# Optimization experiments

Hardware: AMD Instinct MI355X
Metric: run time of the kernel (lower is better)

The kernel has to match this reference:

```python
import jax, jax.numpy as jnp
import numpy as np

# Model dims (eval mode: dropout off, no gate noise, no KV cache, start_pos=0)
B, T, C = 2, 2048, 1024
H, KV = 16, 4
HD = C // H            # 64
E, K = 8, 2            # n_experts, active_experts
FE, FS = 1024, 2048    # expert_inter_dim, shared inter_dim
EPS = 1e-6
BASE = 10000.0


def setup_inputs() -> dict:
    key = jax.random.key(0)
    ks = jax.random.split(key, 15)
    s = 0.02
    f32 = jnp.float32
    return {
        'x': jax.random.normal(ks[0], (B, T, C), f32),
        'norm1_w': jnp.ones((C,), f32),
        'norm2_w': jnp.ones((C,), f32),
        'wq': jax.random.normal(ks[1], (C, H * HD), f32) * s,
        'wk': jax.random.normal(ks[2], (C, KV * HD), f32) * s,
        'wv': jax.random.normal(ks[3], (C, KV * HD), f32) * s,
        'wo': jax.random.normal(ks[4], (H * HD, C), f32) * s,
        'gate_w': jax.random.normal(ks[5], (C, E), f32) * s,
        'exp_w1': jax.random.normal(ks[6], (E, C, FE), f32) * s,
        'exp_w2': jax.random.normal(ks[7], (E, C, FE), f32) * s,
        'exp_wp': jax.random.normal(ks[8], (E, FE, C), f32) * s,
        'sh_w1': jax.random.normal(ks[9], (C, FS), f32) * s,
        'sh_w2': jax.random.normal(ks[10], (C, FS), f32) * s,
        'sh_wp': jax.random.normal(ks[11], (FS, C), f32) * s,
    }


def _rms(x, w):
    return x * jax.lax.rsqrt(jnp.mean(x * x, -1, keepdims=True) + EPS) * w


def _rope_table(t, hd):
    freqs = 1.0 / (BASE ** (jnp.arange(0, hd, 2, dtype=jnp.float32) / hd))
    ang = jnp.outer(jnp.arange(t, dtype=jnp.float32), freqs)  # (T, hd/2)
    return jnp.stack([jnp.cos(ang), jnp.sin(ang)], -1)        # (T, hd/2, 2)


def _apply_rope(x, fc):
    # x: (B, T, nH, hd); fc: (T, hd/2, 2)
    xr = x.reshape(*x.shape[:-1], -1, 2)
    cos = fc[None, :, None, :, 0]
    sin = fc[None, :, None, :, 1]
    out = jnp.stack([xr[..., 0] * cos - xr[..., 1] * sin,
                     xr[..., 1] * cos + xr[..., 0] * sin], -1)
    return out.reshape(x.shape).astype(x.dtype)


def reference(x, norm1_w, norm2_w, wq, wk, wv, wo, gate_w,
              exp_w1, exp_w2, exp_wp, sh_w1, sh_w2, sh_wp):
    fc = _rope_table(T, HD)
    # --- GQA attention with RoPE ---
    h1 = _rms(x, norm1_w)
    q = (h1 @ wq).reshape(B, T, H, HD)
    k = (h1 @ wk).reshape(B, T, KV, HD)
    v = (h1 @ wv).reshape(B, T, KV, HD)
    q = _apply_rope(q, fc)
    k = _apply_rope(k, fc)
    rep = H // KV
    k = jnp.repeat(k, rep, axis=2)  # (B,T,H,HD)
    v = jnp.repeat(v, rep, axis=2)
    scores = jnp.einsum('bqhd,bkhd->bhqk', q, k) / jnp.sqrt(jnp.float32(HD))
    mask = jnp.where(jnp.tril(jnp.ones((T, T), bool)), 0.0, -1e9).astype(scores.dtype)
    att = jax.nn.softmax(scores + mask, axis=-1)
    o = jnp.einsum('bhqk,bkhd->bqhd', att, v).reshape(B, T, C) @ wo
    x1 = x + o
    # --- MoE block (top-k gate, dense masked combine == gather/scatter math) ---
    h2 = _rms(x1, norm2_w).reshape(-1, C)  # (N, C), N = B*T
    gate_logits = h2 @ gate_w              # (N, E)
    p = jax.nn.softmax(gate_logits, axis=-1)
    topw, topi = jax.lax.top_k(p, K)       # values == gather(p, indices)
    comb = jnp.sum(jax.nn.one_hot(topi, E, dtype=p.dtype) * topw[..., None], axis=1)  # (N, E)
    he = jax.nn.silu(jnp.einsum('nc,ecf->enf', h2, exp_w1)) * jnp.einsum('nc,ecf->enf', h2, exp_w2)
    ye = jnp.einsum('enf,efc->enc', he, exp_wp)
    y = jnp.einsum('enc,ne->nc', ye, comb)
    z = (jax.nn.silu(h2 @ sh_w1) * (h2 @ sh_w2)) @ sh_wp
    out = x1 + (y + z).reshape(B, T, C)
    return out, gate_logits
```

## Files before the change

kernel.cpp:

```cpp
#include <hip/hip_runtime.h>
#include <hip/hip_bf16.h>

#define TB 2
#define TT 2048
#define TC 1024
#define TH 16
#define TKV 4
#define THD 64
#define TE 8
#define TFE 1024
#define TFS 2048
#define NTOK 4096
#define NSLOT 8192

typedef __attribute__((ext_vector_type(4))) float f32x4;
typedef __attribute__((ext_vector_type(8))) short s16x8;

__device__ __forceinline__ float bf2f(short s) {
    unsigned int u = ((unsigned int)(unsigned short)s) << 16;
    return __builtin_bit_cast(float, u);
}
__device__ __forceinline__ short f2bf(float f) {
    unsigned int u = __builtin_bit_cast(unsigned int, f);
    u = u + 0x7fffu + ((u >> 16) & 1u);
    return (short)(u >> 16);
}

__device__ __forceinline__ void gl_lds16(const void* g, void* l) {
    __builtin_amdgcn_global_load_lds((const __attribute__((address_space(1))) void*)g,
                                     (__attribute__((address_space(3))) void*)l,
                                     16, 0, 0);
}

__global__ __launch_bounds__(256) void k_transp(const float* __restrict__ in,
                                                short* __restrict__ out,
                                                int R, int Cd,
                                                size_t bs_in, size_t bs_out) {
    __shared__ float tile[32][33];
    const float* ip = in + bs_in * blockIdx.z;
    short* op = out + bs_out * blockIdx.z;
    int tx = threadIdx.x & 31, ty = threadIdx.x >> 5;
    int r0 = blockIdx.y * 32, c0 = blockIdx.x * 32;
    #pragma unroll
    for (int r = ty; r < 32; r += 8)
        tile[r][tx] = ip[(size_t)(r0 + r) * Cd + c0 + tx];
    __syncthreads();
    #pragma unroll
    for (int r = ty; r < 32; r += 8)
        op[(size_t)(c0 + r) * R + r0 + tx] = f2bf(tile[tx][r]);
}

__global__ __launch_bounds__(256) void k_transp_v(const short* __restrict__ qkv,
                                                  short* __restrict__ v_t) {
    __shared__ short tile[32][33];
    int z = blockIdx.z;
    int b = z >> 2, kvh = z & 3;
    const short* ip = qkv + (size_t)b * TT * 1536 + 1280 + kvh * 64;
    short* op = v_t + (size_t)z * THD * TT;
    int tx = threadIdx.x & 31, ty = threadIdx.x >> 5;
    int t0 = blockIdx.y * 32, d0 = blockIdx.x * 32;
    #pragma unroll
    for (int r = ty; r < 32; r += 8)
        tile[r][tx] = ip[(size_t)(t0 + r) * 1536 + d0 + tx];
    __syncthreads();
    #pragma unroll
    for (int r = ty; r < 32; r += 8)
        op[(size_t)(d0 + r) * TT + t0 + tx] = tile[tx][r];
}

__global__ void k_rope_table(float* __restrict__ rope) {
    int idx = blockIdx.x * 256 + threadIdx.x;
    if (idx >= TT * 32) return;
    int t = idx >> 5, i = idx & 31;
    float freq = expf(-(float)i * (1.0f / 32.0f) * 9.210340371976184f);
    float ang = (float)t * freq;
    rope[idx * 2 + 0] = cosf(ang);
    rope[idx * 2 + 1] = sinf(ang);
}

__global__ __launch_bounds__(256) void k_rmsnorm(const float* __restrict__ x,
                                                 const float* __restrict__ w,
                                                 short* __restrict__ out) {
    int row = blockIdx.x, t = threadIdx.x;
    float4 v = ((const float4*)(x + (size_t)row * TC))[t];
    float ss = v.x * v.x + v.y * v.y + v.z * v.z + v.w * v.w;
    #pragma unroll
    for (int off = 32; off; off >>= 1) ss += __shfl_xor(ss, off);
    __shared__ float red[4];
    if ((t & 63) == 0) red[t >> 6] = ss;
    __syncthreads();
    float rs = rsqrtf((red[0] + red[1] + red[2] + red[3]) * (1.0f / 1024.0f) + 1e-6f);
    float4 wv = ((const float4*)w)[t];
    short4 o;
    o.x = f2bf(v.x * rs * wv.x);
    o.y = f2bf(v.y * rs * wv.y);
    o.z = f2bf(v.z * rs * wv.z);
    o.w = f2bf(v.w * rs * wv.w);
    ((short4*)(out + (size_t)row * TC))[t] = o;
}

template <int EPI>
__global__ __launch_bounds__(256) void k_gemm128(const short* __restrict__ A,
                                                 const short* __restrict__ Bt,
                                                 void* __restrict__ outp,
                                                 const float* __restrict__ resid,
                                                 int M, int N, int K) {
    __shared__ short As[128 * 32];
    __shared__ short Bs[128 * 32];
    int tid = threadIdx.x;
    int brow = blockIdx.y * 128, bcol = blockIdx.x * 128;
    int wid = tid >> 6, lane = tid & 63;
    int wr = wid >> 1, wc = wid & 1, g = lane >> 4, c = lane & 15;
    int srow = wid * 32 + (lane >> 2);
    int scol = (lane & 3) * 8;
    const short* Ag0 = A + (size_t)(brow + srow) * K + scol;
    const short* Ag1 = A + (size_t)(brow + srow + 16) * K + scol;
    const short* Bg0 = Bt + (size_t)(bcol + srow) * K + scol;
    const short* Bg1 = Bt + (size_t)(bcol + srow + 16) * K + scol;
    int loff = __builtin_amdgcn_readfirstlane(wid * 2048);
    char* Al0 = (char*)As + loff;
    char* Bl0 = (char*)Bs + loff;
    f32x4 acc[4][4] = {};
    for (int kk = 0; kk < K; kk += 32) {
        __syncthreads();
        gl_lds16(Ag0 + kk, Al0);
        gl_lds16(Ag1 + kk, Al0 + 1024);
        gl_lds16(Bg0 + kk, Bl0);
        gl_lds16(Bg1 + kk, Bl0 + 1024);
        __syncthreads();
        s16x8 af[4], bf[4];
        #pragma unroll
        for (int m = 0; m < 4; m++) af[m] = *(const s16x8*)(As + (wr * 64 + m * 16 + c) * 32 + g * 8);
        #pragma unroll
        for (int n = 0; n < 4; n++) bf[n] = *(const s16x8*)(Bs + (wc * 64 + n * 16 + c) * 32 + g * 8);
        #pragma unroll
        for (int m = 0; m < 4; m++)
            #pragma unroll
            for (int n = 0; n < 4; n++)
                acc[m][n] = __builtin_amdgcn_mfma_f32_16x16x32_bf16(af[m], bf[n], acc[m][n], 0, 0, 0);
    }
    #pragma unroll
    for (int m = 0; m < 4; m++)
        #pragma unroll
        for (int n = 0; n < 4; n++)
            #pragma unroll
            for (int j = 0; j < 4; j++) {
                int row = brow + wr * 64 + m * 16 + g * 4 + j;
                int col = bcol + wc * 64 + n * 16 + c;
                float v = acc[m][n][j];
                if (EPI == 0)
                    ((short*)outp)[(size_t)row * N + col] = f2bf(v);
                else
                    ((float*)outp)[(size_t)row * N + col] = v + resid[(size_t)row * N + col];
            }
}

__global__ void k_rope_apply(const short* __restrict__ qkv,
                             const float* __restrict__ rope,
                             short* __restrict__ q_r,
                             short* __restrict__ k_r) {
    int idx = blockIdx.x * 256 + threadIdx.x;
    if (idx >= NTOK * 640) return;
    int row = idx / 640;
    int p = idx - row * 640;
    int b = row >> 11, t = row & 2047;
    const short* src = qkv + (size_t)row * 1536;
    if (p < 512) {
        int h = p >> 5, i = p & 31;
        float x0 = bf2f(src[h * 64 + 2 * i]);
        float x1 = bf2f(src[h * 64 + 2 * i + 1]);
        float cs = rope[(t * 32 + i) * 2], sn = rope[(t * 32 + i) * 2 + 1];
        size_t o = ((size_t)(b * TH + h) * TT + t) * THD + 2 * i;
        q_r[o]     = f2bf(x0 * cs - x1 * sn);
        q_r[o + 1] = f2bf(x1 * cs + x0 * sn);
    } else {
        int pk = p - 512;
        int kv = pk >> 5, i = pk & 31;
        float x0 = bf2f(src[1024 + kv * 64 + 2 * i]);
        float x1 = bf2f(src[1024 + kv * 64 + 2 * i + 1]);
        float cs = rope[(t * 32 + i) * 2], sn = rope[(t * 32 + i) * 2 + 1];
        size_t o = ((size_t)(b * TKV + kv) * TT + t) * THD + 2 * i;
        k_r[o]     = f2bf(x0 * cs - x1 * sn);
        k_r[o + 1] = f2bf(x1 * cs + x0 * sn);
    }
}

__global__ __launch_bounds__(256) void k_attn(const short* __restrict__ q_r,
                                              const short* __restrict__ k_r,
                                              const short* __restrict__ v_t,
                                              short* __restrict__ attn_o) {
    int qb = (TT / 64 - 1) - blockIdx.x;
    int bh = blockIdx.y;
    int b = bh >> 4, h = bh & 15, kv = h >> 2;
    int tid = threadIdx.x;
    int w = tid >> 6, lane = tid & 63, g = lane >> 4, c = lane & 15;
    int qrow = qb * 64 + w * 16;

    const short* qp = q_r + ((size_t)(b * TH + h) * TT + qrow) * THD;
    const short* kp = k_r + ((size_t)(b * TKV + kv) * TT) * THD;
    const short* vp = v_t + ((size_t)(b * TKV + kv) * THD) * TT;

    s16x8 aq[2];
    aq[0] = *(const s16x8*)(qp + c * THD + g * 8);
    aq[1] = *(const s16x8*)(qp + c * THD + 32 + g * 8);

    f32x4 o[4] = {};
    float m[4]  = {-1e30f, -1e30f, -1e30f, -1e30f};
    float lsum[4] = {0.f, 0.f, 0.f, 0.f};

    __shared__ short pbuf[4][16 * 64];
    short* pb = &pbuf[w][0];

    s16x8 kcur[8], knext[8], vf[8];
    #pragma unroll
    for (int nt = 0; nt < 4; nt++) {
        kcur[nt * 2]     = *(const s16x8*)(kp + (nt * 16 + c) * THD + g * 8);
        kcur[nt * 2 + 1] = *(const s16x8*)(kp + (nt * 16 + c) * THD + 32 + g * 8);
    }

    for (int kt = 0; kt <= qb; ++kt) {
        #pragma unroll
        for (int nt = 0; nt < 4; nt++) {
            vf[nt * 2]     = *(const s16x8*)(vp + (size_t)(nt * 16 + c) * TT + kt * 64 + g * 8);
            vf[nt * 2 + 1] = *(const s16x8*)(vp + (size_t)(nt * 16 + c) * TT + kt * 64 + 32 + g * 8);
        }
        {
            int ktn = kt < qb ? kt + 1 : kt;
            const short* kpn = kp + (size_t)ktn * 64 * THD;
            #pragma unroll
            for (int nt = 0; nt < 4; nt++) {
                knext[nt * 2]     = *(const s16x8*)(kpn + (nt * 16 + c) * THD + g * 8);
                knext[nt * 2 + 1] = *(const s16x8*)(kpn + (nt * 16 + c) * THD + 32 + g * 8);
            }
        }
        f32x4 S[4] = {};
        #pragma unroll
        for (int nt = 0; nt < 4; nt++) {
            S[nt] = __builtin_amdgcn_mfma_f32_16x16x32_bf16(aq[0], kcur[nt * 2], S[nt], 0, 0, 0);
            S[nt] = __builtin_amdgcn_mfma_f32_16x16x32_bf16(aq[1], kcur[nt * 2 + 1], S[nt], 0, 0, 0);
        }
        #pragma unroll
        for (int nt = 0; nt < 4; nt++)
            #pragma unroll
            for (int j = 0; j < 4; j++) {
                float s = S[nt][j] * 0.125f;
                if (kt == qb) {
                    int kpos = nt * 16 + c;
                    int qpos = w * 16 + g * 4 + j;
                    if (kpos > qpos) s = -1e30f;
                }
                S[nt][j] = s;
            }
        float mn[4];
        #pragma unroll
        for (int j = 0; j < 4; j++) {
            mn[j] = fmaxf(fmaxf(S[0][j], S[1][j]), fmaxf(S[2][j], S[3][j]));
            mn[j] = fmaxf(mn[j], __shfl_xor(mn[j], 1));
            mn[j] = fmaxf(mn[j], __shfl_xor(mn[j], 2));
            mn[j] = fmaxf(mn[j], __shfl_xor(mn[j], 4));
            mn[j] = fmaxf(mn[j], __shfl_xor(mn[j], 8));
        }
        #pragma unroll
        for (int j = 0; j < 4; j++) {
            float mnew = fmaxf(m[j], mn[j]);
            float al = __expf(m[j] - mnew);
            m[j] = mnew;
            lsum[j] *= al;
            #pragma unroll
            for (int nt = 0; nt < 4; nt++) o[nt][j] *= al;
        }
        float rsum[4] = {0.f, 0.f, 0.f, 0.f};
        #pragma unroll
        for (int nt = 0; nt < 4; nt++)
            #pragma unroll
            for (int j = 0; j < 4; j++) {
                float pv = __expf(S[nt][j] - m[j]);
                S[nt][j] = pv;
                rsum[j] += pv;
            }
        #pragma unroll
        for (int j = 0; j < 4; j++) {
            rsum[j] += __shfl_xor(rsum[j], 1);
            rsum[j] += __shfl_xor(rsum[j], 2);
            rsum[j] += __shfl_xor(rsum[j], 4);
            rsum[j] += __shfl_xor(rsum[j], 8);
            lsum[j] += rsum[j];
        }
        #pragma unroll
        for (int nt = 0; nt < 4; nt++)
            #pragma unroll
            for (int j = 0; j < 4; j++) {
                int row = g * 4 + j;
                pb[(row * 64 + nt * 16 + c) ^ ((row & 7) << 3)] = f2bf(S[nt][j]);
            }
        s16x8 pa0 = *(const s16x8*)(pb + ((c * 64 + g * 8) ^ ((c & 7) << 3)));
        s16x8 pa1 = *(const s16x8*)(pb + ((c * 64 + 32 + g * 8) ^ ((c & 7) << 3)));
        #pragma unroll
        for (int nt = 0; nt < 4; nt++) {
            o[nt] = __builtin_amdgcn_mfma_f32_16x16x32_bf16(pa0, vf[nt * 2], o[nt], 0, 0, 0);
            o[nt] = __builtin_amdgcn_mfma_f32_16x16x32_bf16(pa1, vf[nt * 2 + 1], o[nt], 0, 0, 0);
        }
        #pragma unroll
        for (int i = 0; i < 8; i++) kcur[i] = knext[i];
    }
    float inv[4];
    #pragma unroll
    for (int j = 0; j < 4; j++) inv[j] = 1.0f / lsum[j];
    #pragma unroll
    for (int nt = 0; nt < 4; nt++)
        #pragma unroll
        for (int j = 0; j < 4; j++) {
            float v = o[nt][j] * inv[j];
            attn_o[(size_t)(b * TT + qb * 64 + w * 16 + g * 4 + j) * TC + h * THD + nt * 16 + c] = f2bf(v);
        }
    (void)qrow;
}

__global__ __launch_bounds__(256) void k_gate(const float* __restrict__ x1,
                                              const float* __restrict__ n2w,
                                              const float* __restrict__ gate_w,
                                              float* __restrict__ gl,
                                              int* __restrict__ cnt,
                                              int* __restrict__ te,
                                              int* __restrict__ tls,
                                              float* __restrict__ tw) {
    int w = threadIdx.x >> 6, lane = threadIdx.x & 63;
    int n = blockIdx.x * 4 + w;
    const float* xp = x1 + (size_t)n * TC;
    float ss = 0.f;
    for (int i = lane; i < TC; i += 64) { float v = xp[i]; ss += v * v; }
    #pragma unroll
    for (int off = 32; off; off >>= 1) ss += __shfl_xor(ss, off);
    float rs = rsqrtf(ss * (1.0f / 1024.0f) + 1e-6f);
    int e = lane & 7, ch = lane >> 3;
    float acc = 0.f;
    for (int i = 0; i < 128; i++) {
        int cc = ch * 128 + i;
        acc += xp[cc] * rs * n2w[cc] * gate_w[(size_t)cc * TE + e];
    }
    acc += __shfl_xor(acc, 8);
    acc += __shfl_xor(acc, 16);
    acc += __shfl_xor(acc, 32);
    float logit = acc;
    if (lane < 8) gl[(size_t)n * TE + lane] = logit;
    float mx = logit;
    mx = fmaxf(mx, __shfl_xor(mx, 1)); mx = fmaxf(mx, __shfl_xor(mx, 2)); mx = fmaxf(mx, __shfl_xor(mx, 4));
    float ex = __expf(logit - mx);
    float sm = ex;
    sm += __shfl_xor(sm, 1); sm += __shfl_xor(sm, 2); sm += __shfl_xor(sm, 4);
    float pp = ex / sm;
    float m1 = pp;
    m1 = fmaxf(m1, __shfl_xor(m1, 1)); m1 = fmaxf(m1, __shfl_xor(m1, 2)); m1 = fmaxf(m1, __shfl_xor(m1, 4));
    int cand = (pp == m1) ? e : 8;
    int e0 = cand;
    e0 = min(e0, __shfl_xor(e0, 1)); e0 = min(e0, __shfl_xor(e0, 2)); e0 = min(e0, __shfl_xor(e0, 4));
    float p2 = (e == e0) ? -1.0f : pp;
    float m2 = p2;
    m2 = fmaxf(m2, __shfl_xor(m2, 1)); m2 = fmaxf(m2, __shfl_xor(m2, 2)); m2 = fmaxf(m2, __shfl_xor(m2, 4));
    int cand2 = (p2 == m2) ? e : 8;
    int e1 = cand2;
    e1 = min(e1, __shfl_xor(e1, 1)); e1 = min(e1, __shfl_xor(e1, 2)); e1 = min(e1, __shfl_xor(e1, 4));
    if (lane == 0) {
        int ls0 = atomicAdd(&cnt[e0], 1);
        int ls1 = atomicAdd(&cnt[e1], 1);
        te[n * 2] = e0; te[n * 2 + 1] = e1;
        tls[n * 2] = ls0; tls[n * 2 + 1] = ls1;
        tw[n * 2] = m1; tw[n * 2 + 1] = m2;
    }
}

__global__ void k_prefix(const int* __restrict__ cnt, int* __restrict__ basep) {
    if (threadIdx.x == 0) {
        int s = 0;
        for (int e = 0; e < TE; e++) { basep[e] = s; s += cnt[e]; }
    }
}

__global__ void k_scatter(const int* __restrict__ te, const int* __restrict__ tls,
                          const float* __restrict__ tw, const int* __restrict__ basep,
                          int* __restrict__ tlist, float* __restrict__ slotw,
                          int* __restrict__ sot) {
    int n = blockIdx.x * 256 + threadIdx.x;
    if (n >= NTOK) return;
    int s0 = basep[te[n * 2]] + tls[n * 2];
    int s1 = basep[te[n * 2 + 1]] + tls[n * 2 + 1];
    tlist[s0] = n; tlist[s1] = n;
    slotw[s0] = tw[n * 2]; slotw[s1] = tw[n * 2 + 1];
    sot[n * 2] = s0; sot[n * 2 + 1] = s1;
}

template <int GATHER>
__global__ __launch_bounds__(256) void k_dual(const short* __restrict__ A,
                                              const short* __restrict__ B1t,
                                              const short* __restrict__ B2t,
                                              short* __restrict__ Out,
                                              const int* __restrict__ cnt,
                                              const int* __restrict__ basep,
                                              const int* __restrict__ tlist,
                                              const float* __restrict__ slotw,
                                              size_t wrows, int ldout, int K) {
    int e = blockIdx.z;
    int mt = blockIdx.y, nt = blockIdx.x;
    int ce = 0, base = 0;
    if (GATHER) {
        ce = cnt[e];
        if (mt * 128 >= ce) return;
        base = basep[e];
    }
    __shared__ short As[128 * 32];
    __shared__ short B1s[64 * 32];
    __shared__ short B2s[64 * 32];
    int tid = threadIdx.x, wid = tid >> 6, lane = tid & 63;
    int wr = wid >> 1, wc = wid & 1, g = lane >> 4, c = lane & 15;
    int srow = wid * 32 + (lane >> 2);
    int scol = (lane & 3) * 8;
    size_t arow0, arow1;
    if (GATHER) {
        int l0 = mt * 128 + srow;      if (l0 >= ce) l0 = ce - 1;
        int l1 = mt * 128 + srow + 16; if (l1 >= ce) l1 = ce - 1;
        arow0 = (size_t)tlist[base + l0];
        arow1 = (size_t)tlist[base + l1];
    } else {
        arow0 = (size_t)(mt * 128 + srow);
        arow1 = arow0 + 16;
    }
    const short* Ag0 = A + arow0 * (size_t)K + scol;
    const short* Ag1 = A + arow1 * (size_t)K + scol;
    int brow_s = wid * 16 + (lane >> 2);
    const short* B1g = B1t + ((size_t)e * wrows + (size_t)(nt * 64 + brow_s)) * K + scol;
    const short* B2g = B2t + ((size_t)e * wrows + (size_t)(nt * 64 + brow_s)) * K + scol;
    int loffA = __builtin_amdgcn_readfirstlane(wid * 2048);
    int loffB = __builtin_amdgcn_readfirstlane(wid * 1024);
    char* Al = (char*)As + loffA;
    char* B1l = (char*)B1s + loffB;
    char* B2l = (char*)B2s + loffB;
    f32x4 a1[4][2] = {}, a2[4][2] = {};
    for (int kk = 0; kk < K; kk += 32) {
        __syncthreads();
        gl_lds16(Ag0 + kk, Al);
        gl_lds16(Ag1 + kk, Al + 1024);
        gl_lds16(B1g + kk, B1l);
        gl_lds16(B2g + kk, B2l);
        __syncthreads();
        s16x8 af[4], b1[2], b2[2];
        #pragma unroll
        for (int m_ = 0; m_ < 4; m_++) af[m_] = *(const s16x8*)(As + (wr * 64 + m_ * 16 + c) * 32 + g * 8);
        #pragma unroll
        for (int n = 0; n < 2; n++) {
            b1[n] = *(const s16x8*)(B1s + (wc * 32 + n * 16 + c) * 32 + g * 8);
            b2[n] = *(const s16x8*)(B2s + (wc * 32 + n * 16 + c) * 32 + g * 8);
        }
        #pragma unroll
        for (int m_ = 0; m_ < 4; m_++)
            #pragma unroll
            for (int n = 0; n < 2; n++) {
                a1[m_][n] = __builtin_amdgcn_mfma_f32_16x16x32_bf16(af[m_], b1[n], a1[m_][n], 0, 0, 0);
                a2[m_][n] = __builtin_amdgcn_mfma_f32_16x16x32_bf16(af[m_], b2[n], a2[m_][n], 0, 0, 0);
            }
    }
    #pragma unroll
    for (int m_ = 0; m_ < 4; m_++)
        #pragma unroll
        for (int n = 0; n < 2; n++)
            #pragma unroll
            for (int j = 0; j < 4; j++) {
                int lrow = mt * 128 + wr * 64 + m_ * 16 + g * 4 + j;
                if (GATHER && lrow >= ce) continue;
                int col = nt * 64 + wc * 32 + n * 16 + c;
                float g1 = a1[m_][n][j], g2 = a2[m_][n][j];
                float v = g1 / (1.0f + __expf(-g1)) * g2;
                size_t orow = GATHER ? (size_t)(base + lrow) : (size_t)lrow;
                if (GATHER) v *= slotw[base + lrow];
                Out[orow * (size_t)ldout + col] = f2bf(v);
            }
}

__global__ __launch_bounds__(256) void k_moe2(const short* __restrict__ he,
                                              const short* __restrict__ Wpt,
                                              short* __restrict__ ye,
                                              const int* __restrict__ cnt,
                                              const int* __restrict__ basep) {
    int e = blockIdx.z;
    int ce = cnt[e];
    int mt = blockIdx.y;
    if (mt * 128 >= ce) return;
    int base = basep[e];
    int nt = blockIdx.x;
    __shared__ short As[128 * 32];
    __shared__ short Bs[128 * 32];
    int tid = threadIdx.x, wid = tid >> 6, lane = tid & 63;
    int wr = wid >> 1, wc = wid & 1, g = lane >> 4, c = lane & 15;
    int srow = wid * 32 + (lane >> 2);
    int scol = (lane & 3) * 8;
    const short* Ag0 = he + (size_t)(base + mt * 128 + srow) * TFE + scol;
    const short* Ag1 = Ag0 + (size_t)16 * TFE;
    const short* Bg0 = Wpt + ((size_t)e * 1024 + nt * 128 + srow) * TFE + scol;
    const short* Bg1 = Bg0 + (size_t)16 * TFE;
    int loff = __builtin_amdgcn_readfirstlane(wid * 2048);
    char* Al = (char*)As + loff;
    char* Bl = (char*)Bs + loff;
    f32x4 acc[4][4] = {};
    for (int kk = 0; kk < TFE; kk += 32) {
        __syncthreads();
        gl_lds16(Ag0 + kk, Al);
        gl_lds16(Ag1 + kk, Al + 1024);
        gl_lds16(Bg0 + kk, Bl);
        gl_lds16(Bg1 + kk, Bl + 1024);
        __syncthreads();
        s16x8 af[4], bf[4];
        #pragma unroll
        for (int m = 0; m < 4; m++) af[m] = *(const s16x8*)(As + (wr * 64 + m * 16 + c) * 32 + g * 8);
        #pragma unroll
        for (int n = 0; n < 4; n++) bf[n] = *(const s16x8*)(Bs + (wc * 64 + n * 16 + c) * 32 + g * 8);
        #pragma unroll
        for (int m = 0; m < 4; m++)
            #pragma unroll
            for (int n = 0; n < 4; n++)
                acc[m][n] = __builtin_amdgcn_mfma_f32_16x16x32_bf16(af[m], bf[n], acc[m][n], 0, 0, 0);
    }
    #pragma unroll
    for (int m = 0; m < 4; m++)
        #pragma unroll
        for (int n = 0; n < 4; n++)
            #pragma unroll
            for (int j = 0; j < 4; j++) {
                int lrow = mt * 128 + wr * 64 + m * 16 + g * 4 + j;
                if (lrow >= ce) continue;
                int col = nt * 128 + wc * 64 + n * 16 + c;
                ye[(size_t)(base + lrow) * TC + col] = f2bf(acc[m][n][j]);
            }
}

__global__ __launch_bounds__(256) void k_final(const short* __restrict__ A,
                                               const short* __restrict__ Bt,
                                               const float* __restrict__ x1,
                                               const short* __restrict__ ye,
                                               const int* __restrict__ sot,
                                               float* __restrict__ outp) {
    __shared__ short As[128 * 32];
    __shared__ short Bs[128 * 32];
    const int K = TFS;
    int tid = threadIdx.x;
    int brow = blockIdx.y * 128, bcol = blockIdx.x * 128;
    int wid = tid >> 6, lane = tid & 63;
    int wr = wid >> 1, wc = wid & 1, g = lane >> 4, c = lane & 15;
    int srow = wid * 32 + (lane >> 2);
    int scol = (lane & 3) * 8;
    const short* Ag0 = A + (size_t)(brow + srow) * K + scol;
    const short* Ag1 = A + (size_t)(brow + srow + 16) * K + scol;
    const short* Bg0 = Bt + (size_t)(bcol + srow) * K + scol;
    const short* Bg1 = Bt + (size_t)(bcol + srow + 16) * K + scol;
    int loff = __builtin_amdgcn_readfirstlane(wid * 2048);
    char* Al = (char*)As + loff;
    char* Bl = (char*)Bs + loff;
    f32x4 acc[4][4] = {};
    for (int kk = 0; kk < K; kk += 32) {
        __syncthreads();
        gl_lds16(Ag0 + kk, Al);
        gl_lds16(Ag1 + kk, Al + 1024);
        gl_lds16(Bg0 + kk, Bl);
        gl_lds16(Bg1 + kk, Bl + 1024);
        __syncthreads();
        s16x8 af[4], bf[4];
        #pragma unroll
        for (int m = 0; m < 4; m++) af[m] = *(const s16x8*)(As + (wr * 64 + m * 16 + c) * 32 + g * 8);
        #pragma unroll
        for (int n = 0; n < 4; n++) bf[n] = *(const s16x8*)(Bs + (wc * 64 + n * 16 + c) * 32 + g * 8);
        #pragma unroll
        for (int m = 0; m < 4; m++)
            #pragma unroll
            for (int n = 0; n < 4; n++)
                acc[m][n] = __builtin_amdgcn_mfma_f32_16x16x32_bf16(af[m], bf[n], acc[m][n], 0, 0, 0);
    }
    #pragma unroll
    for (int m = 0; m < 4; m++)
        #pragma unroll
        for (int n = 0; n < 4; n++)
            #pragma unroll
            for (int j = 0; j < 4; j++) {
                int row = brow + wr * 64 + m * 16 + g * 4 + j;
                int col = bcol + wc * 64 + n * 16 + c;
                int s0 = sot[row * 2], s1 = sot[row * 2 + 1];
                float v = acc[m][n][j] + x1[(size_t)row * TC + col]
                        + bf2f(ye[(size_t)s0 * TC + col]) + bf2f(ye[(size_t)s1 * TC + col]);
                outp[(size_t)row * TC + col] = v;
            }
}

extern "C" void kernel_launch(void* const* d_in, const int* in_sizes, int n_in,
                              void* d_out, int out_size, void* d_ws, size_t ws_size,
                              hipStream_t stream) {
    const float* x     = (const float*)d_in[0];
    const float* n1w   = (const float*)d_in[1];
    const float* n2w   = (const float*)d_in[2];
    const float* wq    = (const float*)d_in[3];
    const float* wk    = (const float*)d_in[4];
    const float* wv    = (const float*)d_in[5];
    const float* wo    = (const float*)d_in[6];
    const float* gatew = (const float*)d_in[7];
    const float* ew1   = (const float*)d_in[8];
    const float* ew2   = (const float*)d_in[9];
    const float* ewp   = (const float*)d_in[10];
    const float* sw1   = (const float*)d_in[11];
    const float* sw2   = (const float*)d_in[12];
    const float* swp   = (const float*)d_in[13];
    float* outp = (float*)d_out;

    char* p = (char*)d_ws;
    auto alloc = [&](size_t bytes) -> char* {
        char* r = p;
        p += (bytes + 255) & ~(size_t)255;
        return r;
    };
    short* wqkv_t = (short*)alloc(1536 * 1024 * 2);
    short* wo_t   = (short*)alloc(1024 * 1024 * 2);
    short* ew1_t  = (short*)alloc((size_t)8 * 1024 * 1024 * 2);
    short* ew2_t  = (short*)alloc((size_t)8 * 1024 * 1024 * 2);
    short* ewp_t  = (short*)alloc((size_t)8 * 1024 * 1024 * 2);
    short* sw1_t  = (short*)alloc((size_t)2048 * 1024 * 2);
    short* sw2_t  = (short*)alloc((size_t)2048 * 1024 * 2);
    short* swp_t  = (short*)alloc((size_t)1024 * 2048 * 2);
    short* h1     = (short*)alloc((size_t)NTOK * 1024 * 2);
    short* qkv    = (short*)alloc((size_t)NTOK * 1536 * 2);
    short* q_r    = (short*)alloc((size_t)TB * TH * TT * THD * 2);
    short* k_r    = (short*)alloc((size_t)TB * TKV * TT * THD * 2);
    short* v_t    = (short*)alloc((size_t)TB * TKV * THD * TT * 2);
    short* attn_o = (short*)alloc((size_t)NTOK * 1024 * 2);
    float* x1     = (float*)alloc((size_t)NTOK * 1024 * 4);
    short* h2     = (short*)alloc((size_t)NTOK * 1024 * 2);
    float* rope   = (float*)alloc((size_t)TT * 32 * 2 * 4);
    int*   cnt    = (int*)alloc(256);
    int*   basep  = (int*)alloc(256);
    int*   te     = (int*)alloc((size_t)NTOK * 2 * 4);
    int*   tls    = (int*)alloc((size_t)NTOK * 2 * 4);
    float* tw     = (float*)alloc((size_t)NTOK * 2 * 4);
    int*   tlist  = (int*)alloc((size_t)NSLOT * 4);
    float* slotw  = (float*)alloc((size_t)NSLOT * 4);
    int*   sot    = (int*)alloc((size_t)NTOK * 2 * 4);
    short* he     = (short*)alloc((size_t)NSLOT * TFE * 2);
    short* ye     = (short*)alloc((size_t)NSLOT * TC * 2);
    short* shm    = (short*)alloc((size_t)NTOK * TFS * 2);

    dim3 blk(256);

    k_transp<<<dim3(32, 32, 1), blk, 0, stream>>>(wq, wqkv_t, 1024, 1024, 0, 0);
    k_transp<<<dim3(8, 32, 1), blk, 0, stream>>>(wk, wqkv_t + 1024 * 1024, 1024, 256, 0, 0);
    k_transp<<<dim3(8, 32, 1), blk, 0, stream>>>(wv, wqkv_t + 1280 * 1024, 1024, 256, 0, 0);
    k_transp<<<dim3(32, 32, 1), blk, 0, stream>>>(wo, wo_t, 1024, 1024, 0, 0);
    k_transp<<<dim3(32, 32, 8), blk, 0, stream>>>(ew1, ew1_t, 1024, 1024, 1048576, 1048576);
    k_transp<<<dim3(32, 32, 8), blk, 0, stream>>>(ew2, ew2_t, 1024, 1024, 1048576, 1048576);
    k_transp<<<dim3(32, 32, 8), blk, 0, stream>>>(ewp, ewp_t, 1024, 1024, 1048576, 1048576);
    k_transp<<<dim3(64, 32, 1), blk, 0, stream>>>(sw1, sw1_t, 1024, 2048, 0, 0);
    k_transp<<<dim3(64, 32, 1), blk, 0, stream>>>(sw2, sw2_t, 1024, 2048, 0, 0);
    k_transp<<<dim3(32, 64, 1), blk, 0, stream>>>(swp, swp_t, 2048, 1024, 0, 0);

    k_rope_table<<<(TT * 32 + 255) / 256, blk, 0, stream>>>(rope);

    k_rmsnorm<<<NTOK, blk, 0, stream>>>(x, n1w, h1);
    k_gemm128<0><<<dim3(12, 32), blk, 0, stream>>>(h1, wqkv_t, qkv, nullptr, NTOK, 1536, 1024);
    k_rope_apply<<<(NTOK * 640 + 255) / 256, blk, 0, stream>>>(qkv, rope, q_r, k_r);
    k_transp_v<<<dim3(2, 64, 8), blk, 0, stream>>>(qkv, v_t);

    k_attn<<<dim3(TT / 64, TB * TH), blk, 0, stream>>>(q_r, k_r, v_t, attn_o);

    k_gemm128<1><<<dim3(8, 32), blk, 0, stream>>>(attn_o, wo_t, x1, x, NTOK, 1024, 1024);

    k_rmsnorm<<<NTOK, blk, 0, stream>>>(x1, n2w, h2);

    hipMemsetAsync(cnt, 0, 64, stream);
    k_gate<<<NTOK / 4, blk, 0, stream>>>(x1, n2w, gatew, outp + (size_t)NTOK * TC, cnt, te, tls, tw);
    k_prefix<<<1, 64, 0, stream>>>(cnt, basep);
    k_scatter<<<NTOK / 256, blk, 0, stream>>>(te, tls, tw, basep, tlist, slotw, sot);

    k_dual<1><<<dim3(16, 32, 8), blk, 0, stream>>>(h2, ew1_t, ew2_t, he, cnt, basep, tlist, slotw,
                                                   1024, TFE, 1024);
    k_moe2<<<dim3(8, 32, 8), blk, 0, stream>>>(he, ewp_t, ye, cnt, basep);

    k_dual<0><<<dim3(32, 32, 1), blk, 0, stream>>>(h2, sw1_t, sw2_t, shm, nullptr, nullptr, nullptr,
                                                   nullptr, 0, TFS, 1024);

    k_final<<<dim3(8, 32), blk, 0, stream>>>(shm, swp_t, x1, ye, sot, outp);

    (void)in_sizes; (void)n_in; (void)out_size; (void)ws_size;
}
```

Before: 846.9 us.

## Rewrite attention with 32x32 MFMA, shrink GEMM N-tiles, merge FFN launches

Attention now gives each wave its own 32-query tile. It uses 32x32x16 bf16 MFMAs, keeps probabilities in registers through cvt_pk_bf16 and permlane32_swap instead of an LDS round trip, and raises MFMA issue priority. The dense GEMMs (QKV, Wo, MoE down projection, final) move from 128x128 to 128x64 tiles, doubling the block count to fill more CUs. The MoE up-projection and the shared-expert up-projection are merged into one launch so they overlap. This trades per-block data reuse and makes more early-exiting blocks in the merged grid in exchange for higher occupancy and no LDS traffic in attention.

```diff
diff --git a/kernel.cpp b/kernel.cpp
--- a/kernel.cpp
+++ b/kernel.cpp
@@ -14,6 +14,7 @@
 #define NSLOT 8192
 
 typedef __attribute__((ext_vector_type(4))) float f32x4;
+typedef __attribute__((ext_vector_type(16))) float f32x16;
 typedef __attribute__((ext_vector_type(8))) short s16x8;
 
 __device__ __forceinline__ float bf2f(short s) {
@@ -24,6 +25,11 @@
     unsigned int u = __builtin_bit_cast(unsigned int, f);
     u = u + 0x7fffu + ((u >> 16) & 1u);
     return (short)(u >> 16);
+}
+__device__ __forceinline__ unsigned int cvtpk_bf16(float lo, float hi) {
+    unsigned int r;
+    asm volatile("v_cvt_pk_bf16_f32 %0, %1, %2" : "=v"(r) : "v"(lo), "v"(hi));
+    return r;
 }
 
 __device__ __forceinline__ void gl_lds16(const void* g, void* l) {
@@ -100,53 +106,53 @@
 }
 
 template <int EPI>
-__global__ __launch_bounds__(256) void k_gemm128(const short* __restrict__ A,
-                                                 const short* __restrict__ Bt,
-                                                 void* __restrict__ outp,
-                                                 const float* __restrict__ resid,
-                                                 int M, int N, int K) {
+__global__ __launch_bounds__(256) void k_gemm64(const short* __restrict__ A,
+                                                const short* __restrict__ Bt,
+                                                void* __restrict__ outp,
+                                                const float* __restrict__ resid,
+                                                int M, int N, int K) {
     __shared__ short As[128 * 32];
-    __shared__ short Bs[128 * 32];
+    __shared__ short Bs[64 * 32];
     int tid = threadIdx.x;
-    int brow = blockIdx.y * 128, bcol = blockIdx.x * 128;
+    int brow = blockIdx.y * 128, bcol = blockIdx.x * 64;
     int wid = tid >> 6, lane = tid & 63;
     int wr = wid >> 1, wc = wid & 1, g = lane >> 4, c = lane & 15;
     int srow = wid * 32 + (lane >> 2);
     int scol = (lane & 3) * 8;
     const short* Ag0 = A + (size_t)(brow + srow) * K + scol;
     const short* Ag1 = A + (size_t)(brow + srow + 16) * K + scol;
-    const short* Bg0 = Bt + (size_t)(bcol + srow) * K + scol;
-    const short* Bg1 = Bt + (size_t)(bcol + srow + 16) * K + scol;
-    int loff = __builtin_amdgcn_readfirstlane(wid * 2048);
-    char* Al0 = (char*)As + loff;
-    char* Bl0 = (char*)Bs + loff;
-    f32x4 acc[4][4] = {};
+    int sbrow = wid * 16 + (lane >> 2);
+    const short* Bg = Bt + (size_t)(bcol + sbrow) * K + scol;
+    int loffA = __builtin_amdgcn_readfirstlane(wid * 2048);
+    int loffB = __builtin_amdgcn_readfirstlane(wid * 1024);
+    char* Al = (char*)As + loffA;
+    char* Bl = (char*)Bs + loffB;
+    f32x4 acc[4][2] = {};
     for (int kk = 0; kk < K; kk += 32) {
         __syncthreads();
-        gl_lds16(Ag0 + kk, Al0);
-        gl_lds16(Ag1 + kk, Al0 + 1024);
-        gl_lds16(Bg0 + kk, Bl0);
-        gl_lds16(Bg1 + kk, Bl0 + 1024);
-        __syncthreads();
-        s16x8 af[4], bf[4];
+        gl_lds16(Ag0 + kk, Al);
+        gl_lds16(Ag1 + kk, Al + 1024);
+        gl_lds16(Bg + kk, Bl);
+        __syncthreads();
+        s16x8 af[4], bf[2];
         #pragma unroll
         for (int m = 0; m < 4; m++) af[m] = *(const s16x8*)(As + (wr * 64 + m * 16 + c) * 32 + g * 8);
         #pragma unroll
-        for (int n = 0; n < 4; n++) bf[n] = *(const s16x8*)(Bs + (wc * 64 + n * 16 + c) * 32 + g * 8);
+        for (int n = 0; n < 2; n++) bf[n] = *(const s16x8*)(Bs + (wc * 32 + n * 16 + c) * 32 + g * 8);
         #pragma unroll
         for (int m = 0; m < 4; m++)
             #pragma unroll
-            for (int n = 0; n < 4; n++)
+            for (int n = 0; n < 2; n++)
                 acc[m][n] = __builtin_amdgcn_mfma_f32_16x16x32_bf16(af[m], bf[n], acc[m][n], 0, 0, 0);
     }
     #pragma unroll
     for (int m = 0; m < 4; m++)
         #pragma unroll
-        for (int n = 0; n < 4; n++)
+        for (int n = 0; n < 2; n++)
             #pragma unroll
             for (int j = 0; j < 4; j++) {
                 int row = brow + wr * 64 + m * 16 + g * 4 + j;
-                int col = bcol + wc * 64 + n * 16 + c;
+                int col = bcol + wc * 32 + n * 16 + c;
                 float v = acc[m][n][j];
                 if (EPI == 0)
                     ((short*)outp)[(size_t)row * N + col] = f2bf(v);
@@ -189,131 +195,121 @@
                                               const short* __restrict__ k_r,
                                               const short* __restrict__ v_t,
                                               short* __restrict__ attn_o) {
-    int qb = (TT / 64 - 1) - blockIdx.x;
+    int w = threadIdx.x >> 6, lane = threadIdx.x & 63;
+    int qt = 63 - (blockIdx.x * 4 + w);
+    int qbase = qt * 32;
     int bh = blockIdx.y;
     int b = bh >> 4, h = bh & 15, kv = h >> 2;
-    int tid = threadIdx.x;
-    int w = tid >> 6, lane = tid & 63, g = lane >> 4, c = lane & 15;
-    int qrow = qb * 64 + w * 16;
-
-    const short* qp = q_r + ((size_t)(b * TH + h) * TT + qrow) * THD;
+    int q32 = lane & 31, hi = lane >> 5;
+
+    const short* qp = q_r + ((size_t)(b * TH + h) * TT + qbase) * THD;
     const short* kp = k_r + ((size_t)(b * TKV + kv) * TT) * THD;
     const short* vp = v_t + ((size_t)(b * TKV + kv) * THD) * TT;
 
-    s16x8 aq[2];
-    aq[0] = *(const s16x8*)(qp + c * THD + g * 8);
-    aq[1] = *(const s16x8*)(qp + c * THD + 32 + g * 8);
-
-    f32x4 o[4] = {};
-    float m[4]  = {-1e30f, -1e30f, -1e30f, -1e30f};
-    float lsum[4] = {0.f, 0.f, 0.f, 0.f};
-
-    __shared__ short pbuf[4][16 * 64];
-    short* pb = &pbuf[w][0];
-
-    s16x8 kcur[8], knext[8], vf[8];
-    #pragma unroll
-    for (int nt = 0; nt < 4; nt++) {
-        kcur[nt * 2]     = *(const s16x8*)(kp + (nt * 16 + c) * THD + g * 8);
-        kcur[nt * 2 + 1] = *(const s16x8*)(kp + (nt * 16 + c) * THD + 32 + g * 8);
-    }
-
-    for (int kt = 0; kt <= qb; ++kt) {
-        #pragma unroll
-        for (int nt = 0; nt < 4; nt++) {
-            vf[nt * 2]     = *(const s16x8*)(vp + (size_t)(nt * 16 + c) * TT + kt * 64 + g * 8);
-            vf[nt * 2 + 1] = *(const s16x8*)(vp + (size_t)(nt * 16 + c) * TT + kt * 64 + 32 + g * 8);
-        }
-        {
-            int ktn = kt < qb ? kt + 1 : kt;
-            const short* kpn = kp + (size_t)ktn * 64 * THD;
-            #pragma unroll
-            for (int nt = 0; nt < 4; nt++) {
-                knext[nt * 2]     = *(const s16x8*)(kpn + (nt * 16 + c) * THD + g * 8);
-                knext[nt * 2 + 1] = *(const s16x8*)(kpn + (nt * 16 + c) * THD + 32 + g * 8);
+    s16x8 qf[4];
+    #pragma unroll
+    for (int dc = 0; dc < 4; dc++)
+        qf[dc] = *(const s16x8*)(qp + q32 * THD + dc * 16 + hi * 8);
+
+    f32x16 ot0 = {}, ot1 = {};
+    float mrun = -1e30f, lrun = 0.f;
+    int nkt = (qbase + 95) >> 6;
+
+    for (int kt = 0; kt < nkt; kt++) {
+        int ktb = kt * 64;
+        f32x16 st0 = {}, st1 = {};
+        s16x8 kf0[4], kf1[4];
+        #pragma unroll
+        for (int dc = 0; dc < 4; dc++) {
+            kf0[dc] = *(const s16x8*)(kp + (size_t)(ktb + q32) * THD + dc * 16 + hi * 8);
+            kf1[dc] = *(const s16x8*)(kp + (size_t)(ktb + 32 + q32) * THD + dc * 16 + hi * 8);
+        }
+        s16x8 vf[8];
+        #pragma unroll
+        for (int dt = 0; dt < 2; dt++)
+            #pragma unroll
+            for (int kc = 0; kc < 4; kc++)
+                vf[dt * 4 + kc] = *(const s16x8*)(vp + (size_t)(dt * 32 + q32) * TT + ktb + kc * 16 + hi * 8);
+
+        __builtin_amdgcn_s_setprio(1);
+        #pragma unroll
+        for (int dc = 0; dc < 4; dc++) {
+            st0 = __builtin_amdgcn_mfma_f32_32x32x16_bf16(kf0[dc], qf[dc], st0, 0, 0, 0);
+            st1 = __builtin_amdgcn_mfma_f32_32x32x16_bf16(kf1[dc], qf[dc], st1, 0, 0, 0);
+        }
+        __builtin_amdgcn_s_setprio(0);
+
+        bool domask = (kt == nkt - 1);
+        int qabs = qbase + q32;
+        #pragma unroll
+        for (int r = 0; r < 16; r++) {
+            int kploc = (r & 3) + 8 * (r >> 2) + 4 * hi;
+            float s0 = st0[r] * 0.125f;
+            float s1 = st1[r] * 0.125f;
+            if (domask) {
+                if (ktb + kploc > qabs) s0 = -1e30f;
+                if (ktb + 32 + kploc > qabs) s1 = -1e30f;
             }
-        }
-        f32x4 S[4] = {};
-        #pragma unroll
-        for (int nt = 0; nt < 4; nt++) {
-            S[nt] = __builtin_amdgcn_mfma_f32_16x16x32_bf16(aq[0], kcur[nt * 2], S[nt], 0, 0, 0);
-            S[nt] = __builtin_amdgcn_mfma_f32_16x16x32_bf16(aq[1], kcur[nt * 2 + 1], S[nt], 0, 0, 0);
-        }
-        #pragma unroll
-        for (int nt = 0; nt < 4; nt++)
-            #pragma unroll
-            for (int j = 0; j < 4; j++) {
-                float s = S[nt][j] * 0.125f;
-                if (kt == qb) {
-                    int kpos = nt * 16 + c;
-                    int qpos = w * 16 + g * 4 + j;
-                    if (kpos > qpos) s = -1e30f;
-                }
-                S[nt][j] = s;
-            }
-        float mn[4];
-        #pragma unroll
-        for (int j = 0; j < 4; j++) {
-            mn[j] = fmaxf(fmaxf(S[0][j], S[1][j]), fmaxf(S[2][j], S[3][j]));
-            mn[j] = fmaxf(mn[j], __shfl_xor(mn[j], 1));
-            mn[j] = fmaxf(mn[j], __shfl_xor(mn[j], 2));
-            mn[j] = fmaxf(mn[j], __shfl_xor(mn[j], 4));
-            mn[j] = fmaxf(mn[j], __shfl_xor(mn[j], 8));
-        }
-        #pragma unroll
-        for (int j = 0; j < 4; j++) {
-            float mnew = fmaxf(m[j], mn[j]);
-            float al = __expf(m[j] - mnew);
-            m[j] = mnew;
-            lsum[j] *= al;
-            #pragma unroll
-            for (int nt = 0; nt < 4; nt++) o[nt][j] *= al;
-        }
-        float rsum[4] = {0.f, 0.f, 0.f, 0.f};
-        #pragma unroll
-        for (int nt = 0; nt < 4; nt++)
-            #pragma unroll
-            for (int j = 0; j < 4; j++) {
-                float pv = __expf(S[nt][j] - m[j]);
-                S[nt][j] = pv;
-                rsum[j] += pv;
-            }
-        #pragma unroll
-        for (int j = 0; j < 4; j++) {
-            rsum[j] += __shfl_xor(rsum[j], 1);
-            rsum[j] += __shfl_xor(rsum[j], 2);
-            rsum[j] += __shfl_xor(rsum[j], 4);
-            rsum[j] += __shfl_xor(rsum[j], 8);
-            lsum[j] += rsum[j];
-        }
-        #pragma unroll
-        for (int nt = 0; nt < 4; nt++)
-            #pragma unroll
-            for (int j = 0; j < 4; j++) {
-                int row = g * 4 + j;
-                pb[(row * 64 + nt * 16 + c) ^ ((row & 7) << 3)] = f2bf(S[nt][j]);
-            }
-        s16x8 pa0 = *(const s16x8*)(pb + ((c * 64 + g * 8) ^ ((c & 7) << 3)));
-        s16x8 pa1 = *(const s16x8*)(pb + ((c * 64 + 32 + g * 8) ^ ((c & 7) << 3)));
-        #pragma unroll
-        for (int nt = 0; nt < 4; nt++) {
-            o[nt] = __builtin_amdgcn_mfma_f32_16x16x32_bf16(pa0, vf[nt * 2], o[nt], 0, 0, 0);
-            o[nt] = __builtin_amdgcn_mfma_f32_16x16x32_bf16(pa1, vf[nt * 2 + 1], o[nt], 0, 0, 0);
-        }
-        #pragma unroll
-        for (int i = 0; i < 8; i++) kcur[i] = knext[i];
-    }
-    float inv[4];
-    #pragma unroll
-    for (int j = 0; j < 4; j++) inv[j] = 1.0f / lsum[j];
-    #pragma unroll
-    for (int nt = 0; nt < 4; nt++)
-        #pragma unroll
-        for (int j = 0; j < 4; j++) {
-            float v = o[nt][j] * inv[j];
-            attn_o[(size_t)(b * TT + qb * 64 + w * 16 + g * 4 + j) * TC + h * THD + nt * 16 + c] = f2bf(v);
-        }
-    (void)qrow;
+            st0[r] = s0; st1[r] = s1;
+        }
+        float pm = st0[0];
+        #pragma unroll
+        for (int r = 1; r < 16; r++) pm = fmaxf(pm, st0[r]);
+        #pragma unroll
+        for (int r = 0; r < 16; r++) pm = fmaxf(pm, st1[r]);
+        pm = fmaxf(pm, __shfl_xor(pm, 32));
+        float mnew = fmaxf(mrun, pm);
+        float al = __expf(mrun - mnew);
+        mrun = mnew;
+        float rs = 0.f;
+        #pragma unroll
+        for (int r = 0; r < 16; r++) {
+            float e0 = __expf(st0[r] - mnew); st0[r] = e0; rs += e0;
+            float e1 = __expf(st1[r] - mnew); st1[r] = e1; rs += e1;
+        }
+        rs += __shfl_xor(rs, 32);
+        lrun = lrun * al + rs;
+        #pragma unroll
+        for (int r = 0; r < 16; r++) { ot0[r] *= al; ot1[r] *= al; }
+
+        unsigned int w0[8], w1[8];
+        #pragma unroll
+        for (int j = 0; j < 8; j++) {
+            w0[j] = cvtpk_bf16(st0[2 * j], st0[2 * j + 1]);
+            w1[j] = cvtpk_bf16(st1[2 * j], st1[2 * j + 1]);
+        }
+        s16x8 pf[4];
+        #pragma unroll
+        for (int kc = 0; kc < 4; kc++) {
+            unsigned int* ww = (kc < 2) ? w0 : w1;
+            int kcl = kc & 1;
+            unsigned int x0 = ww[4 * kcl + 0], y0 = ww[4 * kcl + 2];
+            unsigned int x1 = ww[4 * kcl + 1], y1 = ww[4 * kcl + 3];
+            asm volatile("v_permlane32_swap_b32 %0, %1" : "+v"(x0), "+v"(y0));
+            asm volatile("v_permlane32_swap_b32 %0, %1" : "+v"(x1), "+v"(y1));
+            unsigned int fr[4] = {x0, x1, y0, y1};
+            pf[kc] = __builtin_bit_cast(s16x8, *(ulong2*)fr);
+        }
+        __builtin_amdgcn_s_setprio(1);
+        #pragma unroll
+        for (int kc = 0; kc < 4; kc++) {
+            ot0 = __builtin_amdgcn_mfma_f32_32x32x16_bf16(vf[kc], pf[kc], ot0, 0, 0, 0);
+            ot1 = __builtin_amdgcn_mfma_f32_32x32x16_bf16(vf[4 + kc], pf[kc], ot1, 0, 0, 0);
+        }
+        __builtin_amdgcn_s_setprio(0);
+    }
+    float inv = 1.0f / lrun;
+    short* orow = attn_o + (size_t)(b * TT + qbase + q32) * TC + h * THD;
+    #pragma unroll
+    for (int s = 0; s < 4; s++) {
+        short4 v0, v1;
+        v0.x = f2bf(ot0[4 * s + 0] * inv); v0.y = f2bf(ot0[4 * s + 1] * inv);
+        v0.z = f2bf(ot0[4 * s + 2] * inv); v0.w = f2bf(ot0[4 * s + 3] * inv);
+        v1.x = f2bf(ot1[4 * s + 0] * inv); v1.y = f2bf(ot1[4 * s + 1] * inv);
+        v1.z = f2bf(ot1[4 * s + 2] * inv); v1.w = f2bf(ot1[4 * s + 3] * inv);
+        *(short4*)(orow + 8 * s + 4 * hi) = v0;
+        *(short4*)(orow + 32 + 8 * s + 4 * hi) = v1;
+    }
 }
 
 __global__ __launch_bounds__(256) void k_gate(const float* __restrict__ x1,
@@ -389,33 +385,37 @@
     sot[n * 2] = s0; sot[n * 2 + 1] = s1;
 }
 
-template <int GATHER>
-__global__ __launch_bounds__(256) void k_dual(const short* __restrict__ A,
-                                              const short* __restrict__ B1t,
-                                              const short* __restrict__ B2t,
-                                              short* __restrict__ Out,
-                                              const int* __restrict__ cnt,
-                                              const int* __restrict__ basep,
-                                              const int* __restrict__ tlist,
-                                              const float* __restrict__ slotw,
-                                              size_t wrows, int ldout, int K) {
-    int e = blockIdx.z;
-    int mt = blockIdx.y, nt = blockIdx.x;
+__global__ __launch_bounds__(256) void k_ffn(const short* __restrict__ A,
+                                             const short* __restrict__ eB1,
+                                             const short* __restrict__ eB2,
+                                             const short* __restrict__ sB1,
+                                             const short* __restrict__ sB2,
+                                             short* __restrict__ he,
+                                             short* __restrict__ shm,
+                                             const int* __restrict__ cnt,
+                                             const int* __restrict__ basep,
+                                             const int* __restrict__ tlist,
+                                             const float* __restrict__ slotw) {
+    int z = blockIdx.z;
+    int moe = (z < 8);
+    int nt = blockIdx.x, mt = blockIdx.y;
     int ce = 0, base = 0;
-    if (GATHER) {
-        ce = cnt[e];
+    if (moe) {
+        if (nt >= 16) return;
+        ce = cnt[z];
         if (mt * 128 >= ce) return;
-        base = basep[e];
+        base = basep[z];
     }
     __shared__ short As[128 * 32];
     __shared__ short B1s[64 * 32];
     __shared__ short B2s[64 * 32];
     int tid = threadIdx.x, wid = tid >> 6, lane = tid & 63;
     int wr = wid >> 1, wc = wid & 1, g = lane >> 4, c = lane & 15;
+    const int K = TC;
     int srow = wid * 32 + (lane >> 2);
     int scol = (lane & 3) * 8;
     size_t arow0, arow1;
-    if (GATHER) {
+    if (moe) {
         int l0 = mt * 128 + srow;      if (l0 >= ce) l0 = ce - 1;
         int l1 = mt * 128 + srow + 16; if (l1 >= ce) l1 = ce - 1;
         arow0 = (size_t)tlist[base + l0];
@@ -426,9 +426,16 @@
     }
     const short* Ag0 = A + arow0 * (size_t)K + scol;
     const short* Ag1 = A + arow1 * (size_t)K + scol;
-    int brow_s = wid * 16 + (lane >> 2);
-    const short* B1g = B1t + ((size_t)e * wrows + (size_t)(nt * 64 + brow_s)) * K + scol;
-    const short* B2g = B2t + ((size_t)e * wrows + (size_t)(nt * 64 + brow_s)) * K + scol;
+    int sbrow = wid * 16 + (lane >> 2);
+    const short* B1g;
+    const short* B2g;
+    if (moe) {
+        B1g = eB1 + ((size_t)z * TFE + (size_t)(nt * 64 + sbrow)) * K + scol;
+        B2g = eB2 + ((size_t)z * TFE + (size_t)(nt * 64 + sbrow)) * K + scol;
+    } else {
+        B1g = sB1 + (size_t)(nt * 64 + sbrow) * K + scol;
+        B2g = sB2 + (size_t)(nt * 64 + sbrow) * K + scol;
+    }
     int loffA = __builtin_amdgcn_readfirstlane(wid * 2048);
     int loffB = __builtin_amdgcn_readfirstlane(wid * 1024);
     char* Al = (char*)As + loffA;
@@ -465,13 +472,16 @@
             #pragma unroll
             for (int j = 0; j < 4; j++) {
                 int lrow = mt * 128 + wr * 64 + m_ * 16 + g * 4 + j;
-                if (GATHER && lrow >= ce) continue;
+                if (moe && lrow >= ce) continue;
                 int col = nt * 64 + wc * 32 + n * 16 + c;
                 float g1 = a1[m_][n][j], g2 = a2[m_][n][j];
                 float v = g1 / (1.0f + __expf(-g1)) * g2;
-                size_t orow = GATHER ? (size_t)(base + lrow) : (size_t)lrow;
-                if (GATHER) v *= slotw[base + lrow];
-                Out[orow * (size_t)ldout + col] = f2bf(v);
+                if (moe) {
+                    v *= slotw[base + lrow];
+                    he[(size_t)(base + lrow) * TFE + col] = f2bf(v);
+                } else {
+                    shm[(size_t)lrow * TFS + col] = f2bf(v);
+                }
             }
 }
 
@@ -487,46 +497,46 @@
     int base = basep[e];
     int nt = blockIdx.x;
     __shared__ short As[128 * 32];
-    __shared__ short Bs[128 * 32];
+    __shared__ short Bs[64 * 32];
     int tid = threadIdx.x, wid = tid >> 6, lane = tid & 63;
     int wr = wid >> 1, wc = wid & 1, g = lane >> 4, c = lane & 15;
     int srow = wid * 32 + (lane >> 2);
     int scol = (lane & 3) * 8;
     const short* Ag0 = he + (size_t)(base + mt * 128 + srow) * TFE + scol;
     const short* Ag1 = Ag0 + (size_t)16 * TFE;
-    const short* Bg0 = Wpt + ((size_t)e * 1024 + nt * 128 + srow) * TFE + scol;
-    const short* Bg1 = Bg0 + (size_t)16 * TFE;
-    int loff = __builtin_amdgcn_readfirstlane(wid * 2048);
-    char* Al = (char*)As + loff;
-    char* Bl = (char*)Bs + loff;
-    f32x4 acc[4][4] = {};
+    int sbrow = wid * 16 + (lane >> 2);
+    const short* Bg = Wpt + ((size_t)e * 1024 + nt * 64 + sbrow) * TFE + scol;
+    int loffA = __builtin_amdgcn_readfirstlane(wid * 2048);
+    int loffB = __builtin_amdgcn_readfirstlane(wid * 1024);
+    char* Al = (char*)As + loffA;
+    char* Bl = (char*)Bs + loffB;
+    f32x4 acc[4][2] = {};
     for (int kk = 0; kk < TFE; kk += 32) {
         __syncthreads();
         gl_lds16(Ag0 + kk, Al);
         gl_lds16(Ag1 + kk, Al + 1024);
-        gl_lds16(Bg0 + kk, Bl);
-        gl_lds16(Bg1 + kk, Bl + 1024);
-        __syncthreads();
-        s16x8 af[4], bf[4];
+        gl_lds16(Bg + kk, Bl);
+        __syncthreads();
+        s16x8 af[4], bf[2];
         #pragma unroll
         for (int m = 0; m < 4; m++) af[m] = *(const s16x8*)(As + (wr * 64 + m * 16 + c) * 32 + g * 8);
         #pragma unroll
-        for (int n = 0; n < 4; n++) bf[n] = *(const s16x8*)(Bs + (wc * 64 + n * 16 + c) * 32 + g * 8);
+        for (int n = 0; n < 2; n++) bf[n] = *(const s16x8*)(Bs + (wc * 32 + n * 16 + c) * 32 + g * 8);
         #pragma unroll
         for (int m = 0; m < 4; m++)
             #pragma unroll
-            for (int n = 0; n < 4; n++)
+            for (int n = 0; n < 2; n++)
                 acc[m][n] = __builtin_amdgcn_mfma_f32_16x16x32_bf16(af[m], bf[n], acc[m][n], 0, 0, 0);
     }
     #pragma unroll
     for (int m = 0; m < 4; m++)
         #pragma unroll
-        for (int n = 0; n < 4; n++)
+        for (int n = 0; n < 2; n++)
             #pragma unroll
             for (int j = 0; j < 4; j++) {
                 int lrow = mt * 128 + wr * 64 + m * 16 + g * 4 + j;
                 if (lrow >= ce) continue;
-                int col = nt * 128 + wc * 64 + n * 16 + c;
+                int col = nt * 64 + wc * 32 + n * 16 + c;
                 ye[(size_t)(base + lrow) * TC + col] = f2bf(acc[m][n][j]);
             }
 }
@@ -538,48 +548,48 @@
                                                const int* __restrict__ sot,
                                                float* __restrict__ outp) {
     __shared__ short As[128 * 32];
-    __shared__ short Bs[128 * 32];
+    __shared__ short Bs[64 * 32];
     const int K = TFS;
     int tid = threadIdx.x;
-    int brow = blockIdx.y * 128, bcol = blockIdx.x * 128;
+    int brow = blockIdx.y * 128, bcol = blockIdx.x * 64;
     int wid = tid >> 6, lane = tid & 63;
     int wr = wid >> 1, wc = wid & 1, g = lane >> 4, c = lane & 15;
     int srow = wid * 32 + (lane >> 2);
     int scol = (lane & 3) * 8;
     const short* Ag0 = A + (size_t)(brow + srow) * K + scol;
     const short* Ag1 = A + (size_t)(brow + srow + 16) * K + scol;
-    const short* Bg0 = Bt + (size_t)(bcol + srow) * K + scol;
-    const short* Bg1 = Bt + (size_t)(bcol + srow + 16) * K + scol;
-    int loff = __builtin_amdgcn_readfirstlane(wid * 2048);
-    char* Al = (char*)As + loff;
-    char* Bl = (char*)Bs + loff;
-    f32x4 acc[4][4] = {};
+    int sbrow = wid * 16 + (lane >> 2);
+    const short* Bg = Bt + (size_t)(bcol + sbrow) * K + scol;
+    int loffA = __builtin_amdgcn_readfirstlane(wid * 2048);
+    int loffB = __builtin_amdgcn_readfirstlane(wid * 1024);
+    char* Al = (char*)As + loffA;
+    char* Bl = (char*)Bs + loffB;
+    f32x4 acc[4][2] = {};
     for (int kk = 0; kk < K; kk += 32) {
         __syncthreads();
         gl_lds16(Ag0 + kk, Al);
         gl_lds16(Ag1 + kk, Al + 1024);
-        gl_lds16(Bg0 + kk, Bl);
-        gl_lds16(Bg1 + kk, Bl + 1024);
-        __syncthreads();
-        s16x8 af[4], bf[4];
+        gl_lds16(Bg + kk, Bl);
+        __syncthreads();
+        s16x8 af[4], bf[2];
         #pragma unroll
         for (int m = 0; m < 4; m++) af[m] = *(const s16x8*)(As + (wr * 64 + m * 16 + c) * 32 + g * 8);
         #pragma unroll
-        for (int n = 0; n < 4; n++) bf[n] = *(const s16x8*)(Bs + (wc * 64 + n * 16 + c) * 32 + g * 8);
+        for (int n = 0; n < 2; n++) bf[n] = *(const s16x8*)(Bs + (wc * 32 + n * 16 + c) * 32 + g * 8);
         #pragma unroll
         for (int m = 0; m < 4; m++)
             #pragma unroll
-            for (int n = 0; n < 4; n++)
+            for (int n = 0; n < 2; n++)
                 acc[m][n] = __builtin_amdgcn_mfma_f32_16x16x32_bf16(af[m], bf[n], acc[m][n], 0, 0, 0);
     }
     #pragma unroll
     for (int m = 0; m < 4; m++)
         #pragma unroll
-        for (int n = 0; n < 4; n++)
+        for (int n = 0; n < 2; n++)
             #pragma unroll
             for (int j = 0; j < 4; j++) {
                 int row = brow + wr * 64 + m * 16 + g * 4 + j;
-                int col = bcol + wc * 64 + n * 16 + c;
+                int col = bcol + wc * 32 + n * 16 + c;
                 int s0 = sot[row * 2], s1 = sot[row * 2 + 1];
                 float v = acc[m][n][j] + x1[(size_t)row * TC + col]
                         + bf2f(ye[(size_t)s0 * TC + col]) + bf2f(ye[(size_t)s1 * TC + col]);
@@ -657,13 +667,13 @@
     k_rope_table<<<(TT * 32 + 255) / 256, blk, 0, stream>>>(rope);
 
     k_rmsnorm<<<NTOK, blk, 0, stream>>>(x, n1w, h1);
-    k_gemm128<0><<<dim3(12, 32), blk, 0, stream>>>(h1, wqkv_t, qkv, nullptr, NTOK, 1536, 1024);
+    k_gemm64<0><<<dim3(24, 32), blk, 0, stream>>>(h1, wqkv_t, qkv, nullptr, NTOK, 1536, 1024);
     k_rope_apply<<<(NTOK * 640 + 255) / 256, blk, 0, stream>>>(qkv, rope, q_r, k_r);
     k_transp_v<<<dim3(2, 64, 8), blk, 0, stream>>>(qkv, v_t);
 
-    k_attn<<<dim3(TT / 64, TB * TH), blk, 0, stream>>>(q_r, k_r, v_t, attn_o);
-
-    k_gemm128<1><<<dim3(8, 32), blk, 0, stream>>>(attn_o, wo_t, x1, x, NTOK, 1024, 1024);
+    k_attn<<<dim3(16, TB * TH), blk, 0, stream>>>(q_r, k_r, v_t, attn_o);
+
+    k_gemm64<1><<<dim3(16, 32), blk, 0, stream>>>(attn_o, wo_t, x1, x, NTOK, 1024, 1024);
 
     k_rmsnorm<<<NTOK, blk, 0, stream>>>(x1, n2w, h2);
 
@@ -672,14 +682,11 @@
     k_prefix<<<1, 64, 0, stream>>>(cnt, basep);
     k_scatter<<<NTOK / 256, blk, 0, stream>>>(te, tls, tw, basep, tlist, slotw, sot);
 
-    k_dual<1><<<dim3(16, 32, 8), blk, 0, stream>>>(h2, ew1_t, ew2_t, he, cnt, basep, tlist, slotw,
-                                                   1024, TFE, 1024);
-    k_moe2<<<dim3(8, 32, 8), blk, 0, stream>>>(he, ewp_t, ye, cnt, basep);
-
-    k_dual<0><<<dim3(32, 32, 1), blk, 0, stream>>>(h2, sw1_t, sw2_t, shm, nullptr, nullptr, nullptr,
-                                                   nullptr, 0, TFS, 1024);
-
-    k_final<<<dim3(8, 32), blk, 0, stream>>>(shm, swp_t, x1, ye, sot, outp);
+    k_ffn<<<dim3(32, 32, 9), blk, 0, stream>>>(h2, ew1_t, ew2_t, sw1_t, sw2_t, he, shm,
+                                               cnt, basep, tlist, slotw);
+    k_moe2<<<dim3(16, 32, 8), blk, 0, stream>>>(he, ewp_t, ye, cnt, basep);
+
+    k_final<<<dim3(16, 32), blk, 0, stream>>>(shm, swp_t, x1, ye, sot, outp);
 
     (void)in_sizes; (void)n_in; (void)out_size; (void)ws_size;
 }
```

New measurement: 758.5 us. -10.4%, faster.
